# Performance work log

Hardware: AMD Instinct MI355X
Metric: run time of the kernel (lower is better)

The kernel has to match this reference:

```python
import jax, jax.numpy as jnp
import numpy as np
from jax import lax

B, S, I, H, O, T = 8, 1024, 512, 1024, 512, 8
THRESH = 0.5


def setup_inputs() -> dict:
    key = jax.random.key(0)
    k = jax.random.split(key, 5)
    return {
        "x": jax.random.normal(k[0], (B, S, I), dtype=jnp.float32),
        "w1": jax.random.normal(k[1], (H, I), dtype=jnp.float32) * (1.0 / np.sqrt(I)),
        "b1": jax.random.normal(k[2], (H,), dtype=jnp.float32) * 0.01,
        "w2": jax.random.normal(k[3], (O, H), dtype=jnp.float32) * (1.0 / np.sqrt(H)),
        "b2": jax.random.normal(k[4], (O,), dtype=jnp.float32) * 0.01,
    }


def reference(x, w1, b1, w2, b2):
    # x: (B, S, I). Precompute the input current once (same every timestep).
    inp_cur = jnp.einsum("bsi,hi->bsh", x, w1) + b1  # (B, S, H)
    mem1_0 = jnp.zeros((B, S, H), dtype=x.dtype)
    mem2_0 = jnp.zeros((B, S, O), dtype=x.dtype)

    def step(carry, _):
        mem1, mem2 = carry
        mem1 = mem1 + inp_cur
        spike1 = (mem1 > THRESH).astype(x.dtype)
        mem1 = mem1 * (mem1 <= THRESH).astype(x.dtype)  # reset fired neurons
        mem2 = mem2 + jnp.einsum("bsh,oh->bso", spike1, w2) + b2
        spike2 = (mem2 > THRESH).astype(x.dtype)
        mem2 = mem2 * (mem2 <= THRESH).astype(x.dtype)
        return (mem1, mem2), spike2

    _, spikes = lax.scan(step, (mem1_0, mem2_0), None, length=T)  # (T, B, S, O)
    return jnp.moveaxis(spikes, 0, 1)  # stack on dim=1 -> (B, T, S, O)
```

## Files before the change

kernel.cpp:

```cpp
#include <hip/hip_runtime.h>

static constexpr int B_ = 8, S_ = 1024, I_ = 512, H_ = 1024, O_ = 512, T_ = 8;
static constexpr int M_ = B_ * S_;
static constexpr float TH = 0.5f;

__global__ __launch_bounds__(256) void k1(const float* __restrict__ X,
                                          const float* __restrict__ W1,
                                          const float* __restrict__ B1,
                                          unsigned char* __restrict__ SPB) {
  __shared__ float As[16][132];
  __shared__ float Bs[16][68];
  const int tid = threadIdx.x;
  const int tx = tid & 15, ty = tid >> 4;
  const int rowBase = blockIdx.x * 128, colBase = blockIdx.y * 64;
  const int rrA = tid >> 2, kqA = (tid & 3) << 2;

  float acc[8][4];
#pragma unroll
  for (int i = 0; i < 8; ++i)
#pragma unroll
    for (int j = 0; j < 4; ++j) acc[i][j] = 0.f;

  float4 pa0, pa1, pb;
#define K1_LOAD(IT)                                                            \
  {                                                                            \
    pa0 = *(const float4*)&X[(size_t)(rowBase + rrA) * I_ + (IT) * 16 + kqA];  \
    pa1 = *(const float4*)&X[(size_t)(rowBase + 64 + rrA) * I_ + (IT) * 16 + kqA]; \
    pb  = *(const float4*)&W1[(size_t)(colBase + rrA) * I_ + (IT) * 16 + kqA]; \
  }

  K1_LOAD(0);
  for (int it = 0; it < 32; ++it) {
    As[kqA + 0][rrA] = pa0.x; As[kqA + 1][rrA] = pa0.y;
    As[kqA + 2][rrA] = pa0.z; As[kqA + 3][rrA] = pa0.w;
    As[kqA + 0][64 + rrA] = pa1.x; As[kqA + 1][64 + rrA] = pa1.y;
    As[kqA + 2][64 + rrA] = pa1.z; As[kqA + 3][64 + rrA] = pa1.w;
    Bs[kqA + 0][rrA] = pb.x; Bs[kqA + 1][rrA] = pb.y;
    Bs[kqA + 2][rrA] = pb.z; Bs[kqA + 3][rrA] = pb.w;
    __syncthreads();
    if (it + 1 < 32) K1_LOAD(it + 1);
#pragma unroll
    for (int k = 0; k < 16; ++k) {
      float a[8], b[4];
      *(float4*)&a[0] = *(const float4*)&As[k][ty * 8];
      *(float4*)&a[4] = *(const float4*)&As[k][ty * 8 + 4];
      *(float4*)&b[0] = *(const float4*)&Bs[k][tx * 4];
#pragma unroll
      for (int i = 0; i < 8; ++i)
#pragma unroll
        for (int j = 0; j < 4; ++j) acc[i][j] = fmaf(a[i], b[j], acc[i][j]);
    }
    __syncthreads();
  }
#undef K1_LOAD

#pragma unroll
  for (int i = 0; i < 8; ++i) {
    int row = rowBase + ty * 8 + i;
    unsigned char by[4];
#pragma unroll
    for (int j = 0; j < 4; ++j) {
      int col = colBase + tx * 4 + j;
      float c = acc[i][j] + B1[col];
      float m = 0.f;
      unsigned bits = 0;
#pragma unroll
      for (int t = 0; t < 8; ++t) {
        m = m + c;
        bool s = m > TH;
        bits |= (s ? 1u : 0u) << t;
        m = s ? 0.f : m;
      }
      by[j] = (unsigned char)bits;
    }
    uchar4 pk; pk.x = by[0]; pk.y = by[1]; pk.z = by[2]; pk.w = by[3];
    *(uchar4*)&SPB[(size_t)row * H_ + colBase + tx * 4] = pk;
  }
}

__global__ __launch_bounds__(256) void k2f(const unsigned char* __restrict__ SP,
                                           const float* __restrict__ W2,
                                           const float* __restrict__ B2,
                                           float* __restrict__ out, int tg) {
  __shared__ float As[16][132];
  __shared__ float Bs[16][68];
  const int tid = threadIdx.x;
  const int tx = tid & 15, ty = tid >> 4;
  const int rowBase = blockIdx.x * 32, colBase = blockIdx.y * 64;
  const int sr = tid >> 3;
  const int sk = (tid & 7) << 1;
  const int bc = tid >> 2;
  const int bk = (tid & 3) << 2;
  const int tb = tg * 4;

  float tot[2][4][4], cur[2][4][4];
#pragma unroll
  for (int i = 0; i < 2; ++i)
#pragma unroll
    for (int j = 0; j < 4; ++j)
#pragma unroll
      for (int tt = 0; tt < 4; ++tt) { tot[i][j][tt] = 0.f; cur[i][j][tt] = 0.f; }

  unsigned pu;
  float4 pb;
#define K2_LOAD(IT)                                                            \
  {                                                                            \
    pu = *(const unsigned short*)&SP[(size_t)(rowBase + sr) * H_ + (IT) * 16 + sk]; \
    pb = *(const float4*)&W2[(size_t)(colBase + bc) * H_ + (IT) * 16 + bk];    \
  }

  K2_LOAD(0);
  for (int it = 0; it < 64; ++it) {
    if (it == 32) {
#pragma unroll
      for (int i = 0; i < 2; ++i)
#pragma unroll
        for (int j = 0; j < 4; ++j)
#pragma unroll
          for (int tt = 0; tt < 4; ++tt) {
            tot[i][j][tt] += cur[i][j][tt];
            cur[i][j][tt] = 0.f;
          }
    }
    {
      unsigned b0 = pu & 0xFFu, b1v = (pu >> 8) & 0xFFu;
#pragma unroll
      for (int tt = 0; tt < 4; ++tt) {
        As[sk][sr * 4 + tt]     = (float)((b0 >> (tb + tt)) & 1u);
        As[sk + 1][sr * 4 + tt] = (float)((b1v >> (tb + tt)) & 1u);
      }
      Bs[bk + 0][bc] = pb.x; Bs[bk + 1][bc] = pb.y;
      Bs[bk + 2][bc] = pb.z; Bs[bk + 3][bc] = pb.w;
    }
    __syncthreads();
    if (it + 1 < 64) K2_LOAD(it + 1);
#pragma unroll
    for (int k = 0; k < 16; ++k) {
      float4 a0 = *(const float4*)&As[k][(ty * 2) * 4];
      float4 a1 = *(const float4*)&As[k][(ty * 2 + 1) * 4];
      float4 b  = *(const float4*)&Bs[k][tx * 4];
#pragma unroll
      for (int j = 0; j < 4; ++j)
#pragma unroll
        for (int tt = 0; tt < 4; ++tt) {
          cur[0][j][tt] = fmaf((&a0.x)[tt], (&b.x)[j], cur[0][j][tt]);
          cur[1][j][tt] = fmaf((&a1.x)[tt], (&b.x)[j], cur[1][j][tt]);
        }
    }
    __syncthreads();
  }
#undef K2_LOAD

  const int col0 = colBase + tx * 4;
  float4 b2v = *(const float4*)&B2[col0];
#pragma unroll
  for (int i = 0; i < 2; ++i) {
    int row = rowBase + ty * 2 + i;
    int bb = row >> 10;
    int ss = row & (S_ - 1);
    size_t slot4 = (((size_t)bb * T_ + 4) * S_ + ss) * O_ + col0;
    float mcur[4];
    if (tg == 0) {
      mcur[0] = 0.f; mcur[1] = 0.f; mcur[2] = 0.f; mcur[3] = 0.f;
    } else {
      float4 mp = *(const float4*)&out[slot4];
      mcur[0] = mp.x; mcur[1] = mp.y; mcur[2] = mp.z; mcur[3] = mp.w;
    }
#pragma unroll
    for (int tt = 0; tt < 4; ++tt) {
      int t = tb + tt;
      float4 sp;
#pragma unroll
      for (int j = 0; j < 4; ++j) {
        float d = tot[i][j][tt] + cur[i][j][tt];
        float v = (mcur[j] + d) + (&b2v.x)[j];
        bool s = v > TH;
        (&sp.x)[j] = s ? 1.f : 0.f;
        mcur[j] = s ? 0.f : v;
      }
      *(float4*)&out[(((size_t)bb * T_ + t) * S_ + ss) * O_ + col0] = sp;
    }
    if (tg == 0) {
      float4 mn;
      mn.x = mcur[0]; mn.y = mcur[1]; mn.z = mcur[2]; mn.w = mcur[3];
      *(float4*)&out[slot4] = mn;
    }
  }
}

extern "C" void kernel_launch(void* const* d_in, const int* in_sizes, int n_in,
                              void* d_out, int out_size, void* d_ws, size_t ws_size,
                              hipStream_t stream) {
  const float* x  = (const float*)d_in[0];
  const float* w1 = (const float*)d_in[1];
  const float* b1 = (const float*)d_in[2];
  const float* w2 = (const float*)d_in[3];
  const float* b2 = (const float*)d_in[4];
  float* out = (float*)d_out;

  unsigned char* spikeB = (unsigned char*)d_ws;

  k1<<<dim3(M_ / 128, H_ / 64), 256, 0, stream>>>(x, w1, b1, spikeB);
  k2f<<<dim3(M_ / 32, O_ / 64), 256, 0, stream>>>(spikeB, w2, b2, out, 0);
  k2f<<<dim3(M_ / 32, O_ / 64), 256, 0, stream>>>(spikeB, w2, b2, out, 1);
}
```

Before: 842.5 us.

## Process all eight timesteps in one second-stage kernel launch

Replaces the two k2f launches, each covering four timesteps, with a single kernel that covers 16 rows and all 8 timesteps per block. The membrane state stays in registers across all timesteps. This removes the second kernel launch, the second pass over W2 and the spike matrix, and the round trip of the intermediate membrane state through the output buffer. The grid doubles in block count and each block covers fewer rows, so W2 tile reuse across rows per block is lower.

```diff
diff --git a/kernel.cpp b/kernel.cpp
--- a/kernel.cpp
+++ b/kernel.cpp
@@ -78,34 +78,29 @@
   }
 }
 
-__global__ __launch_bounds__(256) void k2f(const unsigned char* __restrict__ SP,
-                                           const float* __restrict__ W2,
-                                           const float* __restrict__ B2,
-                                           float* __restrict__ out, int tg) {
+__global__ __launch_bounds__(256) void k2f8(const unsigned char* __restrict__ SP,
+                                            const float* __restrict__ W2,
+                                            const float* __restrict__ B2,
+                                            float* __restrict__ out) {
   __shared__ float As[16][132];
   __shared__ float Bs[16][68];
   const int tid = threadIdx.x;
   const int tx = tid & 15, ty = tid >> 4;
-  const int rowBase = blockIdx.x * 32, colBase = blockIdx.y * 64;
-  const int sr = tid >> 3;
-  const int sk = (tid & 7) << 1;
-  const int bc = tid >> 2;
-  const int bk = (tid & 3) << 2;
-  const int tb = tg * 4;
+  const int rowBase = blockIdx.x * 16, colBase = blockIdx.y * 64;
+  const int srow = tid & 15, sk = tid >> 4;
+  const int bc = tid >> 2, bk = (tid & 3) << 2;
 
-  float tot[2][4][4], cur[2][4][4];
+  float tot[4][8], cur[4][8];
 #pragma unroll
-  for (int i = 0; i < 2; ++i)
+  for (int j = 0; j < 4; ++j)
 #pragma unroll
-    for (int j = 0; j < 4; ++j)
-#pragma unroll
-      for (int tt = 0; tt < 4; ++tt) { tot[i][j][tt] = 0.f; cur[i][j][tt] = 0.f; }
+    for (int t = 0; t < 8; ++t) { tot[j][t] = 0.f; cur[j][t] = 0.f; }
 
-  unsigned pu;
+  unsigned char pu;
   float4 pb;
 #define K2_LOAD(IT)                                                            \
   {                                                                            \
-    pu = *(const unsigned short*)&SP[(size_t)(rowBase + sr) * H_ + (IT) * 16 + sk]; \
+    pu = SP[(size_t)(rowBase + srow) * H_ + (IT) * 16 + sk];                   \
     pb = *(const float4*)&W2[(size_t)(colBase + bc) * H_ + (IT) * 16 + bk];    \
   }
 
@@ -113,22 +108,14 @@
   for (int it = 0; it < 64; ++it) {
     if (it == 32) {
 #pragma unroll
-      for (int i = 0; i < 2; ++i)
+      for (int j = 0; j < 4; ++j)
 #pragma unroll
-        for (int j = 0; j < 4; ++j)
-#pragma unroll
-          for (int tt = 0; tt < 4; ++tt) {
-            tot[i][j][tt] += cur[i][j][tt];
-            cur[i][j][tt] = 0.f;
-          }
+        for (int t = 0; t < 8; ++t) { tot[j][t] += cur[j][t]; cur[j][t] = 0.f; }
     }
     {
-      unsigned b0 = pu & 0xFFu, b1v = (pu >> 8) & 0xFFu;
 #pragma unroll
-      for (int tt = 0; tt < 4; ++tt) {
-        As[sk][sr * 4 + tt]     = (float)((b0 >> (tb + tt)) & 1u);
-        As[sk + 1][sr * 4 + tt] = (float)((b1v >> (tb + tt)) & 1u);
-      }
+      for (int t = 0; t < 8; ++t)
+        As[sk][srow * 8 + t] = (float)((pu >> t) & 1u);
       Bs[bk + 0][bc] = pb.x; Bs[bk + 1][bc] = pb.y;
       Bs[bk + 2][bc] = pb.z; Bs[bk + 3][bc] = pb.w;
     }
@@ -136,16 +123,15 @@
     if (it + 1 < 64) K2_LOAD(it + 1);
 #pragma unroll
     for (int k = 0; k < 16; ++k) {
-      float4 a0 = *(const float4*)&As[k][(ty * 2) * 4];
-      float4 a1 = *(const float4*)&As[k][(ty * 2 + 1) * 4];
-      float4 b  = *(const float4*)&Bs[k][tx * 4];
+      float a[8], b[4];
+      *(float4*)&a[0] = *(const float4*)&As[k][ty * 8];
+      *(float4*)&a[4] = *(const float4*)&As[k][ty * 8 + 4];
+      *(float4*)&b[0] = *(const float4*)&Bs[k][tx * 4];
 #pragma unroll
       for (int j = 0; j < 4; ++j)
 #pragma unroll
-        for (int tt = 0; tt < 4; ++tt) {
-          cur[0][j][tt] = fmaf((&a0.x)[tt], (&b.x)[j], cur[0][j][tt]);
-          cur[1][j][tt] = fmaf((&a1.x)[tt], (&b.x)[j], cur[1][j][tt]);
-        }
+        for (int t = 0; t < 8; ++t)
+          cur[j][t] = fmaf(a[t], b[j], cur[j][t]);
     }
     __syncthreads();
   }
@@ -153,38 +139,22 @@
 
   const int col0 = colBase + tx * 4;
   float4 b2v = *(const float4*)&B2[col0];
+  const int row = rowBase + ty;
+  const int bb = row >> 10;
+  const int ss = row & (S_ - 1);
+  float m[4] = {0.f, 0.f, 0.f, 0.f};
 #pragma unroll
-  for (int i = 0; i < 2; ++i) {
-    int row = rowBase + ty * 2 + i;
-    int bb = row >> 10;
-    int ss = row & (S_ - 1);
-    size_t slot4 = (((size_t)bb * T_ + 4) * S_ + ss) * O_ + col0;
-    float mcur[4];
-    if (tg == 0) {
-      mcur[0] = 0.f; mcur[1] = 0.f; mcur[2] = 0.f; mcur[3] = 0.f;
-    } else {
-      float4 mp = *(const float4*)&out[slot4];
-      mcur[0] = mp.x; mcur[1] = mp.y; mcur[2] = mp.z; mcur[3] = mp.w;
+  for (int t = 0; t < 8; ++t) {
+    float4 sp;
+#pragma unroll
+    for (int j = 0; j < 4; ++j) {
+      float d = tot[j][t] + cur[j][t];
+      float v = (m[j] + d) + (&b2v.x)[j];
+      bool s = v > TH;
+      (&sp.x)[j] = s ? 1.f : 0.f;
+      m[j] = s ? 0.f : v;
     }
-#pragma unroll
-    for (int tt = 0; tt < 4; ++tt) {
-      int t = tb + tt;
-      float4 sp;
-#pragma unroll
-      for (int j = 0; j < 4; ++j) {
-        float d = tot[i][j][tt] + cur[i][j][tt];
-        float v = (mcur[j] + d) + (&b2v.x)[j];
-        bool s = v > TH;
-        (&sp.x)[j] = s ? 1.f : 0.f;
-        mcur[j] = s ? 0.f : v;
-      }
-      *(float4*)&out[(((size_t)bb * T_ + t) * S_ + ss) * O_ + col0] = sp;
-    }
-    if (tg == 0) {
-      float4 mn;
-      mn.x = mcur[0]; mn.y = mcur[1]; mn.z = mcur[2]; mn.w = mcur[3];
-      *(float4*)&out[slot4] = mn;
-    }
+    *(float4*)&out[(((size_t)bb * T_ + t) * S_ + ss) * O_ + col0] = sp;
   }
 }
 
@@ -201,6 +171,5 @@
   unsigned char* spikeB = (unsigned char*)d_ws;
 
   k1<<<dim3(M_ / 128, H_ / 64), 256, 0, stream>>>(x, w1, b1, spikeB);
-  k2f<<<dim3(M_ / 32, O_ / 64), 256, 0, stream>>>(spikeB, w2, b2, out, 0);
-  k2f<<<dim3(M_ / 32, O_ / 64), 256, 0, stream>>>(spikeB, w2, b2, out, 1);
+  k2f8<<<dim3(M_ / 16, O_ / 64), 256, 0, stream>>>(spikeB, w2, b2, out);
 }
```

Result: faster. 825.2 us (-2.0%).
